# Kernel tuning notes

Hardware: AMD Instinct MI355X
Metric: run time of the kernel (lower is better)

## Reference

```python
import jax, jax.numpy as jnp
import numpy as np
from jax import lax

# Static problem sizes (match input_specs / init_kwargs)
B, V, K = 32, 2048, 40          # events, vertices per event, n_neighbours
F_IN, D, P, FILT = 64, 4, 64, 128  # input feats, n_dimensions, n_propagate, n_filters
N = B * V


def _dense_init(key, fan_in, fan_out):
    return jax.random.normal(key, (fan_in, fan_out), jnp.float32) / np.sqrt(fan_in)


def setup_inputs() -> dict:
    key = jax.random.key(0)
    k0, k1, k2, k3 = jax.random.split(key, 4)
    return {
        "x": jax.random.normal(k0, (N, F_IN), jnp.float32),
        "row_splits": jnp.arange(B + 1, dtype=jnp.int32) * V,
        "W_s": _dense_init(k1, F_IN, D),
        "b_s": jnp.zeros((D,), jnp.float32),
        "W_f": _dense_init(k2, F_IN, P),
        "b_f": jnp.zeros((P,), jnp.float32),
        "W_out": _dense_init(k3, F_IN + 2 * P, FILT),
        "b_out": jnp.zeros((FILT,), jnp.float32),
    }


def _collect_neighbours(coords, feats):
    # coords: [B, V, D], feats: [B, V, P]
    # KNN in learned coordinate space (per event, brute force).
    sq = jnp.sum(coords * coords, axis=-1)                      # [B, V]
    d2 = sq[:, :, None] + sq[:, None, :] - 2.0 * jnp.einsum(
        "bvd,bwd->bvw", coords, coords)                        # [B, V, V]
    _, idx = lax.top_k(-d2, K + 1)                              # self is nearest
    idx = idx[:, :, 1:]                                         # drop self -> [B, V, K]

    gather = jax.vmap(lambda arr, i: arr[i])                    # per-event gather
    nbr_c = gather(coords, idx)                                 # [B, V, K, D]
    nbr_f = gather(feats, idx)                                  # [B, V, K, P]

    # exact squared distance (as in the TF layer) + gaussian-of-linear weight
    dist = jnp.sum((coords[:, :, None, :] - nbr_c) ** 2, axis=-1)  # [B, V, K]
    w = jnp.exp(-jnp.abs(dist * 10.0))[..., None]                  # [B, V, K, 1]

    nf = nbr_f * w                                              # [B, V, K, P]
    return jnp.concatenate([jnp.max(nf, axis=2), jnp.mean(nf, axis=2)], axis=-1)


def reference(x, row_splits, W_s, b_s, W_f, b_f, W_out, b_out):
    coords = (x @ W_s + b_s).reshape(B, V, D)
    feats = (x @ W_f + b_f).reshape(B, V, P)
    collected = _collect_neighbours(coords, feats).reshape(N, 2 * P)
    updated = jnp.concatenate([x, collected], axis=-1)          # [N, F_IN + 2P]
    return jnp.tanh(updated @ W_out + b_out)                    # [N, FILT]
```

## Files before the change

kernel.cpp:

```cpp
#include <hip/hip_runtime.h>
#include <cfloat>

#define BB   32
#define VV   2048
#define KNB  40
#define FIN  64
#define DD   4
#define PP   64
#define NN   (BB*VV)

static __device__ __forceinline__ float fast_tanh(float z) {
    z = fminf(fmaxf(z, -15.f), 15.f);
    float e = __expf(2.f * z);
    return (e - 1.f) / (e + 1.f);
}

static __device__ __forceinline__ float rfl_f(float x) {
    return __uint_as_float(
        (unsigned)__builtin_amdgcn_readfirstlane(__float_as_int(x)));
}

static __device__ __forceinline__ int wave_incl_scan(int x) {
    x += __builtin_amdgcn_update_dpp(0, x, 0x111, 0xf, 0xf, true);
    x += __builtin_amdgcn_update_dpp(0, x, 0x112, 0xf, 0xf, true);
    x += __builtin_amdgcn_update_dpp(0, x, 0x114, 0xf, 0xf, true);
    x += __builtin_amdgcn_update_dpp(0, x, 0x118, 0xf, 0xf, true);
    x += __builtin_amdgcn_update_dpp(0, x, 0x142, 0xa, 0xf, true);
    x += __builtin_amdgcn_update_dpp(0, x, 0x143, 0xc, 0xf, true);
    return x;
}

__global__ __launch_bounds__(256) void k_embed(
    const float* __restrict__ x, const float* __restrict__ Ws,
    const float* __restrict__ bs, const float* __restrict__ Wf,
    const float* __restrict__ bf, float* __restrict__ coords,
    float* __restrict__ feats)
{
    __shared__ float Xs[64][68];
    __shared__ float Wfs[64][64];
    __shared__ float Wss[64][4];
    const int tid  = threadIdx.x;
    const int row0 = blockIdx.x * 64;

    #pragma unroll
    for (int i = 0; i < 4; ++i) {
        const int idx = tid + i * 256;
        const int r   = idx >> 4;
        const int k4  = (idx & 15) << 2;
        float4 v = *(const float4*)(x + (size_t)(row0 + r) * FIN + k4);
        Xs[k4+0][r] = v.x; Xs[k4+1][r] = v.y; Xs[k4+2][r] = v.z; Xs[k4+3][r] = v.w;
        ((float4*)Wfs)[idx] = ((const float4*)Wf)[idx];
    }
    if (tid < 64) *(float4*)Wss[tid] = ((const float4*)Ws)[tid];
    __syncthreads();

    const int tx = tid & 15;
    const int ty = tid >> 4;
    float acc[4][4] = {};
    #pragma unroll 16
    for (int k = 0; k < 64; ++k) {
        float4 a = *(const float4*)&Xs[k][ty * 4];
        float4 b = *(const float4*)&Wfs[k][tx * 4];
        acc[0][0] += a.x*b.x; acc[0][1] += a.x*b.y; acc[0][2] += a.x*b.z; acc[0][3] += a.x*b.w;
        acc[1][0] += a.y*b.x; acc[1][1] += a.y*b.y; acc[1][2] += a.y*b.z; acc[1][3] += a.y*b.w;
        acc[2][0] += a.z*b.x; acc[2][1] += a.z*b.y; acc[2][2] += a.z*b.z; acc[2][3] += a.z*b.w;
        acc[3][0] += a.w*b.x; acc[3][1] += a.w*b.y; acc[3][2] += a.w*b.z; acc[3][3] += a.w*b.w;
    }
    const float4 bfv = *(const float4*)(bf + tx * 4);
    const float ar[4] = {bfv.x, bfv.y, bfv.z, bfv.w};
    #pragma unroll
    for (int i = 0; i < 4; ++i) {
        float4 o = { acc[i][0] + ar[0], acc[i][1] + ar[1],
                     acc[i][2] + ar[2], acc[i][3] + ar[3] };
        *(float4*)(feats + (size_t)(row0 + ty * 4 + i) * PP + tx * 4) = o;
    }

    const int cr = tid >> 2, cc = tid & 3;
    float ca = bs[cc];
    #pragma unroll 16
    for (int k = 0; k < 64; ++k) ca += Xs[k][cr] * Wss[k][cc];
    coords[(size_t)(row0 + cr) * DD + cc] = ca;
}

static __device__ __forceinline__ bool select_collect(
    const unsigned int (&binsW)[8][64], const unsigned int nearmask,
    int* __restrict__ hw, int* __restrict__ cp, const int lane,
    const bool allow_fail)
{
    int4 hv = ((const int4*)hw)[lane];
    const int local = hv.x + hv.y + hv.z + hv.w;
    const int incl  = wave_incl_scan(local);
    if (allow_fail) {
        const int total = __builtin_amdgcn_readlane(incl, 63);
        if (total < KNB) return false;
    }
    const int excl = incl - local;
    const bool pred = (excl < KNB) && (incl >= KNB);
    const unsigned long long m = __ballot(pred);
    const int src = (m == 0ull) ? 0 : ((int)__ffsll(m) - 1);
    int gg = 0, nnb = 0;
    if (pred) {
        const int hh[4] = {hv.x, hv.y, hv.z, hv.w};
        int cacc = excl, found = -1;
        #pragma unroll
        for (int q = 0; q < 4; ++q) {
            if (found < 0 && cacc + hh[q] >= KNB) { found = q; nnb = cacc; }
            cacc += hh[q];
        }
        gg = (lane << 2) + found;
    }
    const int g1  = __builtin_amdgcn_readlane(gg,  src);
    const int nb1 = __builtin_amdgcn_readlane(nnb, src);

    unsigned int bw[8];
    #pragma unroll
    for (int q = 0; q < 8; ++q) bw[q] = binsW[q][lane];

    unsigned int maskA = 0u, maskB = 0u;
    #pragma unroll
    for (int j = 0; j < 32; ++j) {
        const int bb = (int)((bw[j >> 2] >> ((j & 3) * 8)) & 255u);
        if (bb < g1) maskA |= (1u << j);
        else if (bb == g1) maskB |= (1u << j);
    }
    maskB &= nearmask;

    const int packed = __popc(maskA) | (__popc(maskB) << 16);
    const int incl2  = wave_incl_scan(packed);
    const int excl2  = incl2 - packed;
    int baseA = excl2 & 0xFFFF;
    int baseB = nb1 + (excl2 >> 16);
    while (maskA) {
        const int j = __ffs(maskA) - 1; maskA &= maskA - 1;
        cp[baseA++] = lane + (j << 6);
    }
    while (maskB && baseB < KNB) {
        const int j = __ffs(maskB) - 1; maskB &= maskB - 1;
        cp[baseB++] = lane + (j << 6);
    }
    return true;
}

static __device__ __forceinline__ void rebuild_fb(
    const float4* __restrict__ cb4, const float cvx, const float cvy,
    const float cvz, const float cvw, const int jself,
    const int lself, int* __restrict__ hw, unsigned int (&binsW)[8][64],
    unsigned int& nearm, const int lane)
{
    const int4 izero = {0, 0, 0, 0};
    ((int4*)hw)[lane] = izero;
    nearm = 0u;
    #pragma unroll
    for (int q = 0; q < 8; ++q) {
        unsigned int wq = 0u;
        #pragma unroll
        for (int t = 0; t < 4; ++t) {
            const int j = q * 4 + t;
            const float4 cw = cb4[lane + (j << 6)];
            const float dx = cvx - cw.x, dy = cvy - cw.y;
            const float dz = cvz - cw.z, dw = cvw - cw.w;
            float d2 = dx*dx + dy*dy + dz*dz + dw*dw;
            if (j == jself && lane == lself) d2 = FLT_MAX;
            const bool nr = (d2 < 1024.f);
            const int  bb = nr ? (int)(d2 * 0.25f) : 255;
            wq    |= (unsigned int)bb << (t * 8);
            nearm |= (nr ? 1u : 0u) << j;
            if (nr) atomicAdd(&hw[bb], 1);
        }
        binsW[q][lane] = wq;
        __builtin_amdgcn_sched_barrier(0);
    }
}

__global__ __launch_bounds__(256) void k_knn(
    const float* __restrict__ coords, const float* __restrict__ feats,
    float* __restrict__ collected)
{
    __shared__ int hist[4][2][256];
    __shared__ int candP[4][2][KNB];
    __shared__ unsigned int binsT[4][2][8][64];

    const int tid   = threadIdx.x;
    const int lane  = tid & 63;
    const int w     = tid >> 6;
    const int bid   = (int)blockIdx.x;
    const int swz   = ((bid & 7) << 10) + (bid >> 3);
    const int vA    = __builtin_amdgcn_readfirstlane((swz << 3) + (w << 1));
    const int vB    = vA + 1;
    const int batch = vA >> 11;
    const int vlocA = vA & (VV - 1);
    const float4* cb4 = (const float4*)(coords + (size_t)batch * VV * DD);
    const float*  fb  = feats + (size_t)batch * VV * PP;

    const int4 izero = {0, 0, 0, 0};

    const float4 cva = cb4[vlocA];
    const float4 cvb = cb4[vlocA + 1];
    const float cax = rfl_f(cva.x), cay = rfl_f(cva.y);
    const float caz = rfl_f(cva.z), caw = rfl_f(cva.w);
    const float cbx = rfl_f(cvb.x), cby = rfl_f(cvb.y);
    const float cbz = rfl_f(cvb.z), cbw = rfl_f(cvb.w);
    const int jself  = vlocA >> 6;
    const int lselfA = vlocA & 63;
    const int lselfB = lselfA + 1;

    ((int4*)hist[w][0])[lane] = izero;
    ((int4*)hist[w][1])[lane] = izero;

    unsigned int nearA = 0u, nearB = 0u;
    #pragma unroll
    for (int q = 0; q < 8; ++q) {
        unsigned int wqA = 0u, wqB = 0u;
        #pragma unroll
        for (int t = 0; t < 4; ++t) {
            const int j = q * 4 + t;
            const float4 cw = cb4[lane + (j << 6)];
            const float dxA = cax - cw.x, dyA = cay - cw.y;
            const float dzA = caz - cw.z, dwA = caw - cw.w;
            float d2A = dxA*dxA + dyA*dyA + dzA*dzA + dwA*dwA;
            const float dxB = cbx - cw.x, dyB = cby - cw.y;
            const float dzB = cbz - cw.z, dwB = cbw - cw.w;
            float d2B = dxB*dxB + dyB*dyB + dzB*dzB + dwB*dwB;
            if (j == jself) {
                if (lane == lselfA) d2A = FLT_MAX;
                if (lane == lselfB) d2B = FLT_MAX;
            }
            const bool nA = (d2A < 4.f), nB = (d2B < 4.f);
            const int  bA = nA ? (int)(d2A * 64.f) : 255;
            const int  bB = nB ? (int)(d2B * 64.f) : 255;
            wqA   |= (unsigned int)bA << (t * 8);
            wqB   |= (unsigned int)bB << (t * 8);
            nearA |= (nA ? 1u : 0u) << j;
            nearB |= (nB ? 1u : 0u) << j;
            if (nA) atomicAdd(&hist[w][0][bA], 1);
            if (nB) atomicAdd(&hist[w][1][bB], 1);
        }
        binsT[w][0][q][lane] = wqA;
        binsT[w][1][q][lane] = wqB;
        __builtin_amdgcn_sched_barrier(0);
    }

    if (!select_collect(binsT[w][0], nearA, hist[w][0], candP[w][0], lane, true)) {
        rebuild_fb(cb4, cax, cay, caz, caw, jself, lselfA,
                   hist[w][0], binsT[w][0], nearA, lane);
        select_collect(binsT[w][0], nearA, hist[w][0], candP[w][0], lane, false);
    }
    if (!select_collect(binsT[w][1], nearB, hist[w][1], candP[w][1], lane, true)) {
        rebuild_fb(cb4, cbx, cby, cbz, cbw, jself, lselfB,
                   hist[w][1], binsT[w][1], nearB, lane);
        select_collect(binsT[w][1], nearB, hist[w][1], candP[w][1], lane, false);
    }

    #pragma unroll
    for (int r = 0; r < 2; ++r) {
        const float qx = r ? cbx : cax, qy = r ? cby : cay;
        const float qz = r ? cbz : caz, qw = r ? cbw : caw;
        int ireg = 0; float wgt = 0.f;
        if (lane < KNB) {
            ireg = candP[w][r][lane];
            const float4 cw = cb4[ireg];
            const float dx = qx - cw.x, dy = qy - cw.y;
            const float dz = qz - cw.z, dw = qw - cw.w;
            wgt = __expf(-10.f * (dx*dx + dy*dy + dz*dz + dw*dw));
        }
        float mx = -FLT_MAX, sm = 0.f;
        #pragma unroll
        for (int j0 = 0; j0 < KNB; j0 += 20) {
            float fv[20]; float wv[20];
            #pragma unroll
            for (int t = 0; t < 20; ++t) {
                const int si = __builtin_amdgcn_readlane(ireg, j0 + t);
                wv[t] = __uint_as_float(
                    (unsigned int)__builtin_amdgcn_readlane(__float_as_int(wgt), j0 + t));
                fv[t] = fb[(size_t)(si * PP) + lane];
            }
            #pragma unroll
            for (int t = 0; t < 20; ++t) {
                const float nv = fv[t] * wv[t];
                mx = fmaxf(mx, nv);
                sm += nv;
            }
        }
        float* rowp = collected + ((size_t)(vA + r) << 7);
        rowp[lane]      = mx;
        rowp[PP + lane] = sm * (1.f / KNB);
    }
}

__global__ __launch_bounds__(256) void k_out(
    const float* __restrict__ x, const float* __restrict__ collected,
    const float* __restrict__ Wout, const float* __restrict__ bout,
    float* __restrict__ out)
{
    __shared__ float As[16][68];
    __shared__ float Bs[16][128];
    const int tid = threadIdx.x;
    const int tx  = tid & 15;
    const int ty  = tid >> 4;
    const int row0 = blockIdx.x * 64;

    float acc[4][8];
    #pragma unroll
    for (int i = 0; i < 4; ++i)
        #pragma unroll
        for (int j = 0; j < 8; ++j) acc[i][j] = 0.f;

    for (int k0 = 0; k0 < 192; k0 += 16) {
        {
            const int r   = tid >> 2;
            const int kk4 = (tid & 3) << 2;
            const float* src = (k0 < 64)
                ? (x + (size_t)(row0 + r) * FIN + (k0 + kk4))
                : (collected + (size_t)(row0 + r) * 128 + (k0 - 64 + kk4));
            float4 v = *(const float4*)src;
            As[kk4+0][r] = v.x; As[kk4+1][r] = v.y;
            As[kk4+2][r] = v.z; As[kk4+3][r] = v.w;
        }
        #pragma unroll
        for (int rep = 0; rep < 2; ++rep) {
            const int e = (tid + rep * 256) * 4;
            const int kk = e >> 7, c = e & 127;
            *(float4*)&Bs[kk][c] = *(const float4*)(Wout + (size_t)(k0 + kk) * 128 + c);
        }
        __syncthreads();
        #pragma unroll
        for (int kk = 0; kk < 16; ++kk) {
            float4 a  = *(const float4*)&As[kk][ty * 4];
            float4 b0 = *(const float4*)&Bs[kk][tx * 4];
            float4 b1 = *(const float4*)&Bs[kk][64 + tx * 4];
            const float av[4] = {a.x, a.y, a.z, a.w};
            #pragma unroll
            for (int i = 0; i < 4; ++i) {
                acc[i][0] += av[i] * b0.x; acc[i][1] += av[i] * b0.y;
                acc[i][2] += av[i] * b0.z; acc[i][3] += av[i] * b0.w;
                acc[i][4] += av[i] * b1.x; acc[i][5] += av[i] * b1.y;
                acc[i][6] += av[i] * b1.z; acc[i][7] += av[i] * b1.w;
            }
        }
        __syncthreads();
    }

    #pragma unroll
    for (int i = 0; i < 4; ++i) {
        const int row = row0 + ty * 4 + i;
        float4 o0, o1;
        o0.x = fast_tanh(acc[i][0] + bout[tx*4+0]);
        o0.y = fast_tanh(acc[i][1] + bout[tx*4+1]);
        o0.z = fast_tanh(acc[i][2] + bout[tx*4+2]);
        o0.w = fast_tanh(acc[i][3] + bout[tx*4+3]);
        o1.x = fast_tanh(acc[i][4] + bout[64+tx*4+0]);
        o1.y = fast_tanh(acc[i][5] + bout[64+tx*4+1]);
        o1.z = fast_tanh(acc[i][6] + bout[64+tx*4+2]);
        o1.w = fast_tanh(acc[i][7] + bout[64+tx*4+3]);
        *(float4*)(out + (size_t)row * 128 + tx * 4)      = o0;
        *(float4*)(out + (size_t)row * 128 + 64 + tx * 4) = o1;
    }
}

extern "C" void kernel_launch(void* const* d_in, const int* in_sizes, int n_in,
                              void* d_out, int out_size, void* d_ws, size_t ws_size,
                              hipStream_t stream)
{
    const float* x    = (const float*)d_in[0];
    const float* Ws   = (const float*)d_in[2];
    const float* bs   = (const float*)d_in[3];
    const float* Wf   = (const float*)d_in[4];
    const float* bf   = (const float*)d_in[5];
    const float* Wout = (const float*)d_in[6];
    const float* bout = (const float*)d_in[7];
    float* out = (float*)d_out;

    float* coords = (float*)d_ws;
    float* feats  = (float*)((char*)d_ws + (size_t)NN * DD * sizeof(float));
    float* collected = out;

    hipLaunchKernelGGL(k_embed, dim3(NN / 64), dim3(256), 0, stream,
                       x, Ws, bs, Wf, bf, coords, feats);
    hipLaunchKernelGGL(k_knn, dim3(NN / 8), dim3(256), 0, stream,
                       coords, feats, collected);
    hipLaunchKernelGGL(k_out, dim3(NN / 64), dim3(256), 0, stream,
                       x, collected, Wout, bout, out);
}
```

Measured before the change: 285.1 us.

## Rewrite output GEMM with bf16 MFMA 16x16x32 and larger row tiles

The output projection now runs on bf16 MFMA instructions in place of a scalar fp32 shared-memory GEMM. Activations are loaded straight from global memory into MFMA fragments and rounded to bf16 in registers. Each block converts W_out into a bf16 fragment layout in LDS and covers 128 rows with 512 threads. This removes most of the fp32 FMA and LDS traffic, at the cost of bf16 rounding error and a repeated weight conversion in every block.

```diff
diff --git a/kernel.cpp b/kernel.cpp
--- a/kernel.cpp
+++ b/kernel.cpp
@@ -9,6 +9,9 @@
 #define PP   64
 #define NN   (BB*VV)
 
+typedef __attribute__((ext_vector_type(8))) short bf16x8;
+typedef __attribute__((ext_vector_type(4))) float f32x4;
+
 static __device__ __forceinline__ float fast_tanh(float z) {
     z = fminf(fmaxf(z, -15.f), 15.f);
     float e = __expf(2.f * z);
@@ -18,6 +21,11 @@
 static __device__ __forceinline__ float rfl_f(float x) {
     return __uint_as_float(
         (unsigned)__builtin_amdgcn_readfirstlane(__float_as_int(x)));
+}
+
+static __device__ __forceinline__ unsigned int bf16rne(float f) {
+    const unsigned int u = __float_as_uint(f);
+    return (u + 0x7FFFu + ((u >> 16) & 1u)) >> 16;
 }
 
 static __device__ __forceinline__ int wave_incl_scan(int x) {
@@ -186,7 +194,6 @@
     const int bid   = (int)blockIdx.x;
     const int swz   = ((bid & 7) << 10) + (bid >> 3);
     const int vA    = __builtin_amdgcn_readfirstlane((swz << 3) + (w << 1));
-    const int vB    = vA + 1;
     const int batch = vA >> 11;
     const int vlocA = vA & (VV - 1);
     const float4* cb4 = (const float4*)(coords + (size_t)batch * VV * DD);
@@ -287,73 +294,71 @@
     }
 }
 
-__global__ __launch_bounds__(256) void k_out(
+__global__ __launch_bounds__(512) void k_out(
     const float* __restrict__ x, const float* __restrict__ collected,
     const float* __restrict__ Wout, const float* __restrict__ bout,
     float* __restrict__ out)
 {
-    __shared__ float As[16][68];
-    __shared__ float Bs[16][128];
-    const int tid = threadIdx.x;
-    const int tx  = tid & 15;
-    const int ty  = tid >> 4;
-    const int row0 = blockIdx.x * 64;
-
-    float acc[4][8];
-    #pragma unroll
-    for (int i = 0; i < 4; ++i)
-        #pragma unroll
-        for (int j = 0; j < 8; ++j) acc[i][j] = 0.f;
-
-    for (int k0 = 0; k0 < 192; k0 += 16) {
-        {
-            const int r   = tid >> 2;
-            const int kk4 = (tid & 3) << 2;
-            const float* src = (k0 < 64)
-                ? (x + (size_t)(row0 + r) * FIN + (k0 + kk4))
-                : (collected + (size_t)(row0 + r) * 128 + (k0 - 64 + kk4));
-            float4 v = *(const float4*)src;
-            As[kk4+0][r] = v.x; As[kk4+1][r] = v.y;
-            As[kk4+2][r] = v.z; As[kk4+3][r] = v.w;
-        }
-        #pragma unroll
-        for (int rep = 0; rep < 2; ++rep) {
-            const int e = (tid + rep * 256) * 4;
-            const int kk = e >> 7, c = e & 127;
-            *(float4*)&Bs[kk][c] = *(const float4*)(Wout + (size_t)(k0 + kk) * 128 + c);
-        }
-        __syncthreads();
-        #pragma unroll
-        for (int kk = 0; kk < 16; ++kk) {
-            float4 a  = *(const float4*)&As[kk][ty * 4];
-            float4 b0 = *(const float4*)&Bs[kk][tx * 4];
-            float4 b1 = *(const float4*)&Bs[kk][64 + tx * 4];
-            const float av[4] = {a.x, a.y, a.z, a.w};
-            #pragma unroll
-            for (int i = 0; i < 4; ++i) {
-                acc[i][0] += av[i] * b0.x; acc[i][1] += av[i] * b0.y;
-                acc[i][2] += av[i] * b0.z; acc[i][3] += av[i] * b0.w;
-                acc[i][4] += av[i] * b1.x; acc[i][5] += av[i] * b1.y;
-                acc[i][6] += av[i] * b1.z; acc[i][7] += av[i] * b1.w;
-            }
-        }
-        __syncthreads();
-    }
-
-    #pragma unroll
-    for (int i = 0; i < 4; ++i) {
-        const int row = row0 + ty * 4 + i;
-        float4 o0, o1;
-        o0.x = fast_tanh(acc[i][0] + bout[tx*4+0]);
-        o0.y = fast_tanh(acc[i][1] + bout[tx*4+1]);
-        o0.z = fast_tanh(acc[i][2] + bout[tx*4+2]);
-        o0.w = fast_tanh(acc[i][3] + bout[tx*4+3]);
-        o1.x = fast_tanh(acc[i][4] + bout[64+tx*4+0]);
-        o1.y = fast_tanh(acc[i][5] + bout[64+tx*4+1]);
-        o1.z = fast_tanh(acc[i][6] + bout[64+tx*4+2]);
-        o1.w = fast_tanh(acc[i][7] + bout[64+tx*4+3]);
-        *(float4*)(out + (size_t)row * 128 + tx * 4)      = o0;
-        *(float4*)(out + (size_t)row * 128 + 64 + tx * 4) = o1;
+    __shared__ __align__(16) unsigned short Wf[6 * 8 * 64 * 8];
+
+    const int tid  = threadIdx.x;
+    const int lane = tid & 63;
+    const int wv   = tid >> 6;
+    const int row0 = (int)blockIdx.x * 128;
+
+    for (int s = tid; s < 3072; s += 512) {
+        const int l     = s & 63;
+        const int ct    = (s >> 6) & 7;
+        const int ks    = s >> 9;
+        const int kbase = ks * 32 + (l >> 4) * 8;
+        const int col   = ct * 16 + (l & 15);
+        unsigned int pk[4];
+        #pragma unroll
+        for (int p = 0; p < 4; ++p) {
+            const float f0 = Wout[(size_t)(kbase + 2*p)     * 128 + col];
+            const float f1 = Wout[(size_t)(kbase + 2*p + 1) * 128 + col];
+            pk[p] = bf16rne(f0) | (bf16rne(f1) << 16);
+        }
+        uint4 v = {pk[0], pk[1], pk[2], pk[3]};
+        *(uint4*)&Wf[s * 8] = v;
+    }
+    __syncthreads();
+
+    const int arow = row0 + wv * 16 + (lane & 15);
+    const int koff = (lane >> 4) * 8;
+    f32x4 acc[8];
+    #pragma unroll
+    for (int ct = 0; ct < 8; ++ct) acc[ct] = (f32x4){0.f, 0.f, 0.f, 0.f};
+
+    #pragma unroll
+    for (int ks = 0; ks < 6; ++ks) {
+        const float* src = (ks < 2)
+            ? (x         + (size_t)arow * FIN + ks * 32 + koff)
+            : (collected + (size_t)arow * 128 + (ks - 2) * 32 + koff);
+        const float4 a0 = *(const float4*)(src);
+        const float4 a1 = *(const float4*)(src + 4);
+        unsigned int p0 = bf16rne(a0.x) | (bf16rne(a0.y) << 16);
+        unsigned int p1 = bf16rne(a0.z) | (bf16rne(a0.w) << 16);
+        unsigned int p2 = bf16rne(a1.x) | (bf16rne(a1.y) << 16);
+        unsigned int p3 = bf16rne(a1.z) | (bf16rne(a1.w) << 16);
+        uint4 av = {p0, p1, p2, p3};
+        const bf16x8 afrag = *(const bf16x8*)&av;
+        #pragma unroll
+        for (int ct = 0; ct < 8; ++ct) {
+            const bf16x8 bfrag = *(const bf16x8*)&Wf[((ks * 8 + ct) * 64 + lane) * 8];
+            acc[ct] = __builtin_amdgcn_mfma_f32_16x16x32_bf16(
+                          afrag, bfrag, acc[ct], 0, 0, 0);
+        }
+    }
+
+    const int orow0 = row0 + wv * 16 + (lane >> 4) * 4;
+    #pragma unroll
+    for (int ct = 0; ct < 8; ++ct) {
+        const int ocol = ct * 16 + (lane & 15);
+        const float bb = bout[ocol];
+        #pragma unroll
+        for (int i = 0; i < 4; ++i)
+            out[(size_t)(orow0 + i) * 128 + ocol] = fast_tanh(acc[ct][i] + bb);
     }
 }
 
@@ -378,6 +383,6 @@
                        x, Ws, bs, Wf, bf, coords, feats);
     hipLaunchKernelGGL(k_knn, dim3(NN / 8), dim3(256), 0, stream,
                        coords, feats, collected);
-    hipLaunchKernelGGL(k_out, dim3(NN / 64), dim3(256), 0, stream,
+    hipLaunchKernelGGL(k_out, dim3(NN / 128), dim3(512), 0, stream,
                        x, collected, Wout, bout, out);
 }
```

After: 248.9 us. -12.7%, faster.
